# Kernel optimization log

Hardware: AMD Instinct MI355X
Metric: run time of the kernel (lower is better)

## Reference

```python
import jax, jax.numpy as jnp
import numpy as np

N = 50000          # nodes
E = 1_600_000      # edges (avg degree 32)
IN_CH = 256
HID = 256          # 2 * out_channels
OUT_CH = 128


def setup_inputs() -> dict:
    key = jax.random.key(0)
    k = jax.random.split(key, 5)
    x = jax.random.normal(k[0], (N, IN_CH), dtype=jnp.float32)
    edge_index = jax.random.randint(k[1], (2, E), 0, N, dtype=jnp.int64)
    W1 = jax.random.normal(k[2], (IN_CH, HID), dtype=jnp.float32) * 0.05
    b1 = jnp.zeros((HID,), dtype=jnp.float32)
    W2 = jax.random.normal(k[3], (HID, OUT_CH), dtype=jnp.float32) * 0.05
    b2 = jnp.zeros((OUT_CH,), dtype=jnp.float32)
    return {"x": x, "edge_index": edge_index, "W1": W1, "b1": b1, "W2": W2, "b2": b2}


def _gcn_conv(x, src, dst, deg_inv_sqrt, W, b, n_nodes):
    # GCNConv: linear transform, then normalized sum-aggregation over edges
    # (edge list already includes self-loops; deg_inv_sqrt precomputed).
    h = x @ W                                   # [N, F_out]
    norm = deg_inv_sqrt[src] * deg_inv_sqrt[dst]  # [E+N]
    msg = h[src] * norm[:, None]                # gather + scale
    out = jax.ops.segment_sum(msg, dst, num_segments=n_nodes)  # scatter-add
    return out + b


def reference(x, edge_index, W1, b1, W2, b2):
    n = x.shape[0]
    loop = jnp.arange(n, dtype=edge_index.dtype)
    src = jnp.concatenate([edge_index[0], loop])   # with self-loops
    dst = jnp.concatenate([edge_index[1], loop])
    # symmetric degree normalization (edge weight 1, deg over targets)
    deg = jax.ops.segment_sum(jnp.ones_like(dst, dtype=x.dtype), dst, num_segments=n)
    deg_inv_sqrt = jnp.where(deg > 0, jax.lax.rsqrt(deg), 0.0)

    z = _gcn_conv(x, src, dst, deg_inv_sqrt, W1, b1, n)
    z = jax.nn.relu(z)
    z = _gcn_conv(z, src, dst, deg_inv_sqrt, W2, b2, n)

    # decode: gather endpoint embeddings of original edges, dot product
    value = jnp.sum(z[edge_index[0]] * z[edge_index[1]], axis=-1)  # [E]
    return value.reshape(-1)
```

## Files before the change

### kernel.cpp

```cpp
#include <hip/hip_runtime.h>

#define WS_ALIGN(x) (((x) + 255) & ~(size_t)255)

typedef float f4v __attribute__((ext_vector_type(4)));
__device__ inline void nt_store4(float* p, float4 v) {
  __builtin_nontemporal_store(*(f4v*)&v, (f4v*)p);
}

__global__ void k_init_deg(int* deg, int N) {
  int i = blockIdx.x * blockDim.x + threadIdx.x;
  if (i < N) deg[i] = 1;
}

__global__ void k_count(const int* __restrict__ dst, int E, int* __restrict__ deg) {
  int e = blockIdx.x * blockDim.x + threadIdx.x;
  if (e < E) atomicAdd(&deg[dst[e]], 1);
}

__global__ void k_dis(const int* __restrict__ deg, float* __restrict__ dis, int N) {
  int i = blockIdx.x * blockDim.x + threadIdx.x;
  if (i < N) dis[i] = rsqrtf((float)deg[i]);
}

__global__ __launch_bounds__(1024) void k_scan(const int* __restrict__ deg,
                                               int* __restrict__ rowptr,
                                               int* __restrict__ cursor,
                                               int N, int Etot) {
  __shared__ int wsum[16];
  __shared__ int s_carry;
  int tid = threadIdx.x, lane = tid & 63, w = tid >> 6;
  if (tid == 0) { s_carry = 0; rowptr[N] = Etot; }
  __syncthreads();
  for (int base = 0; base < N; base += 4096) {
    int i0 = base + tid * 4;
    int v[4];
    #pragma unroll
    for (int u = 0; u < 4; ++u) {
      int i = i0 + u;
      v[u] = (i < N) ? (deg[i] - 1) : 0;
    }
    int tsum = v[0] + v[1] + v[2] + v[3];
    int sc = tsum;
    #pragma unroll
    for (int off = 1; off < 64; off <<= 1) {
      int t = __shfl_up(sc, off);
      if (lane >= off) sc += t;
    }
    if (lane == 63) wsum[w] = sc;
    __syncthreads();
    if (w == 0 && lane < 16) {
      int xx = wsum[lane];
      #pragma unroll
      for (int off = 1; off < 16; off <<= 1) {
        int t = __shfl_up(xx, off);
        if (lane >= off) xx += t;
      }
      wsum[lane] = xx;
    }
    __syncthreads();
    int woff = (w == 0) ? 0 : wsum[w - 1];
    int excl = s_carry + woff + (sc - tsum);
    #pragma unroll
    for (int u = 0; u < 4; ++u) {
      int i = i0 + u;
      if (i < N) { rowptr[i] = excl; cursor[i] = excl; }
      excl += v[u];
    }
    __syncthreads();
    if (tid == 0) s_carry += wsum[15];
    __syncthreads();
  }
}

__global__ void k_fill_pack(const int* __restrict__ src, const int* __restrict__ dst, int E,
                            int* __restrict__ cursor, unsigned short* __restrict__ csr16,
                            unsigned int* __restrict__ packed) {
  int e = blockIdx.x * blockDim.x + threadIdx.x;
  if (e < E) {
    int s = src[e];
    int d = dst[e];
    packed[e] = (unsigned int)s | ((unsigned int)d << 16);
    int pos = atomicAdd(&cursor[d], 1);
    csr16[pos] = (unsigned short)s;
  }
}

#define BM 128
#define BN 128
#define BK 16
__global__ __launch_bounds__(256) void k_gemm_scale_sm(const float* __restrict__ A,
                                                       const float* __restrict__ B,
                                                       const float* __restrict__ dis,
                                                       float* __restrict__ C,
                                                       int M, int Nc, int K) {
  __shared__ float As[BK][BM];
  __shared__ float Bs[BK][BN];
  int tid = threadIdx.x;
  int block_row = blockIdx.x * BM;
  int block_col = blockIdx.y * BN;
  int tr = (tid >> 4) << 3;
  int tc = (tid & 15) << 3;
  float acc[8][8] = {};
  for (int k0 = 0; k0 < K; k0 += BK) {
    for (int t = tid; t < BM * BK / 4; t += 256) {
      int r = t >> 2;
      int cc = (t & 3) << 2;
      int gr = block_row + r;
      float4 v = {0.f, 0.f, 0.f, 0.f};
      if (gr < M) v = *(const float4*)(A + (size_t)gr * K + k0 + cc);
      As[cc + 0][r] = v.x; As[cc + 1][r] = v.y; As[cc + 2][r] = v.z; As[cc + 3][r] = v.w;
    }
    for (int t = tid; t < BK * BN / 4; t += 256) {
      int r = t >> 5;
      int cc = (t & 31) << 2;
      *(float4*)&Bs[r][cc] = *(const float4*)(B + (size_t)(k0 + r) * Nc + block_col + cc);
    }
    __syncthreads();
    #pragma unroll
    for (int k = 0; k < BK; ++k) {
      float a[8], b[8];
      *(float4*)&a[0] = *(const float4*)&As[k][tr];
      *(float4*)&a[4] = *(const float4*)&As[k][tr + 4];
      *(float4*)&b[0] = *(const float4*)&Bs[k][tc];
      *(float4*)&b[4] = *(const float4*)&Bs[k][tc + 4];
      #pragma unroll
      for (int i = 0; i < 8; ++i)
        #pragma unroll
        for (int j = 0; j < 8; ++j)
          acc[i][j] = fmaf(a[i], b[j], acc[i][j]);
    }
    __syncthreads();
  }
  int col0 = block_col + tc;
  size_t base = ((size_t)(col0 >> 4) * M) * 16 + (col0 & 15);
  for (int i = 0; i < 8; ++i) {
    int gr = block_row + tr + i;
    if (gr >= M) break;
    float s = dis[gr];
    float4 v0 = {acc[i][0] * s, acc[i][1] * s, acc[i][2] * s, acc[i][3] * s};
    float4 v1 = {acc[i][4] * s, acc[i][5] * s, acc[i][6] * s, acc[i][7] * s};
    float* cp = C + base + (size_t)gr * 16;
    *(float4*)cp = v0;
    *(float4*)(cp + 4) = v1;
  }
}

template <int FCH, bool OUTSLICE>
__global__ __launch_bounds__(256) void k_agg_xcd(const float* __restrict__ hs,
                                                 const int* __restrict__ rowptr,
                                                 const unsigned short* __restrict__ csr,
                                                 const float* __restrict__ dis,
                                                 const float* __restrict__ bias,
                                                 float* __restrict__ out,
                                                 int N, int do_relu) {
  const int NSLICE = FCH / 16;
  int bid = blockIdx.x;
  int xcd = bid & 7;
  int wid = threadIdx.x >> 6;
  int lane = threadIdx.x & 63;
  int sub = lane >> 3;
  int epar = (lane >> 2) & 1;
  int c2 = lane & 3;
  int wix = ((bid >> 3) << 2) + wid;
  int wpx = ((int)(gridDim.x >> 3)) << 2;
  int nchunk = (N + 7) >> 3;

  for (int ph = 0; ph < NSLICE / 8; ++ph) {
    int s = xcd + (ph << 3);
    const float* in = hs + (size_t)s * N * 16;
    for (int ch = wix; ch < nchunk; ch += wpx) {
      int node = (ch << 3) + sub;
      bool valid = node < N;
      int b0 = 0, e0 = 0;
      if (valid) { b0 = rowptr[node]; e0 = rowptr[node + 1]; }
      float4 acc = {0.f, 0.f, 0.f, 0.f};
      int j = b0 + epar;
      for (; j + 6 < e0; j += 8) {
        int i0 = csr[j];     int i1 = csr[j + 2];
        int i2 = csr[j + 4]; int i3 = csr[j + 6];
        float4 v0 = *(const float4*)(in + ((size_t)i0 << 4) + (c2 << 2));
        float4 v1 = *(const float4*)(in + ((size_t)i1 << 4) + (c2 << 2));
        float4 v2 = *(const float4*)(in + ((size_t)i2 << 4) + (c2 << 2));
        float4 v3 = *(const float4*)(in + ((size_t)i3 << 4) + (c2 << 2));
        acc.x += (v0.x + v1.x) + (v2.x + v3.x);
        acc.y += (v0.y + v1.y) + (v2.y + v3.y);
        acc.z += (v0.z + v1.z) + (v2.z + v3.z);
        acc.w += (v0.w + v1.w) + (v2.w + v3.w);
      }
      for (; j < e0; j += 2) {
        int idx = csr[j];
        float4 v = *(const float4*)(in + ((size_t)idx << 4) + (c2 << 2));
        acc.x += v.x; acc.y += v.y; acc.z += v.z; acc.w += v.w;
      }
      acc.x += __shfl_xor(acc.x, 4);
      acc.y += __shfl_xor(acc.y, 4);
      acc.z += __shfl_xor(acc.z, 4);
      acc.w += __shfl_xor(acc.w, 4);
      if (valid && epar == 0) {
        float4 self = *(const float4*)(in + ((size_t)node << 4) + (c2 << 2));
        float dn = dis[node];
        int col = (s << 4) + (c2 << 2);
        float4 bv = *(const float4*)(bias + col);
        float4 r;
        r.x = (acc.x + self.x) * dn + bv.x;
        r.y = (acc.y + self.y) * dn + bv.y;
        r.z = (acc.z + self.z) * dn + bv.z;
        r.w = (acc.w + self.w) * dn + bv.w;
        if (do_relu) {
          r.x = fmaxf(r.x, 0.f); r.y = fmaxf(r.y, 0.f);
          r.z = fmaxf(r.z, 0.f); r.w = fmaxf(r.w, 0.f);
        }
        if (OUTSLICE)
          nt_store4(out + (size_t)s * N * 16 + ((size_t)node << 4) + (c2 << 2), r);
        else
          nt_store4(out + (size_t)node * FCH + col, r);
      }
    }
  }
}

__global__ __launch_bounds__(256) void k_decode_xcd4(const float* __restrict__ z,
                                                     const unsigned int* __restrict__ packed,
                                                     float* __restrict__ partial,
                                                     int E, int N) {
  int bid = blockIdx.x;
  int xcd = bid & 7;
  int wid = threadIdx.x >> 6;
  int lane = threadIdx.x & 63;
  int c2 = lane & 3;
  int sub = lane >> 2;
  int wix = ((bid >> 3) << 2) + wid;
  int wpx = ((int)(gridDim.x >> 3)) << 2;
  const float* zc = z + (size_t)xcd * N * 16;
  float* pp = partial + (size_t)xcd * E;

  for (int e0 = wix * 32; e0 < E; e0 += wpx * 32) {
    int eA = e0 + sub;
    int eB = e0 + 16 + sub;
    bool vA = eA < E, vB = eB < E;
    unsigned int pkA = 0, pkB = 0;
    if (vA) pkA = packed[eA];
    if (vB) pkB = packed[eB];
    float pA = 0.f, pB = 0.f;
    if (vA) {
      int a = (int)(pkA & 0xFFFFu), d = (int)(pkA >> 16);
      float4 za = *(const float4*)(zc + ((size_t)a << 4) + (c2 << 2));
      float4 zb = *(const float4*)(zc + ((size_t)d << 4) + (c2 << 2));
      pA = za.x * zb.x + za.y * zb.y + za.z * zb.z + za.w * zb.w;
    }
    if (vB) {
      int a = (int)(pkB & 0xFFFFu), d = (int)(pkB >> 16);
      float4 za = *(const float4*)(zc + ((size_t)a << 4) + (c2 << 2));
      float4 zb = *(const float4*)(zc + ((size_t)d << 4) + (c2 << 2));
      pB = za.x * zb.x + za.y * zb.y + za.z * zb.z + za.w * zb.w;
    }
    pA += __shfl_xor(pA, 1);
    pA += __shfl_xor(pA, 2);
    pB += __shfl_xor(pB, 1);
    pB += __shfl_xor(pB, 2);
    if (c2 == 0) {
      if (vA) pp[eA] = pA;
      if (vB) pp[eB] = pB;
    }
  }
}

__global__ void k_dreduce(const float* __restrict__ partial, float* __restrict__ out, int E) {
  int e = blockIdx.x * 256 + threadIdx.x;
  if (e >= E) return;
  float s = 0.f;
  #pragma unroll
  for (int k = 0; k < 8; ++k) s += partial[(size_t)k * E + e];
  out[e] = s;
}

extern "C" void kernel_launch(void* const* d_in, const int* in_sizes, int n_in,
                              void* d_out, int out_size, void* d_ws, size_t ws_size,
                              hipStream_t stream) {
  const float* x  = (const float*)d_in[0];
  const int* eidx = (const int*)d_in[1];
  const float* W1 = (const float*)d_in[2];
  const float* b1 = (const float*)d_in[3];
  const float* W2 = (const float*)d_in[4];
  const float* b2 = (const float*)d_in[5];
  float* out = (float*)d_out;

  const int IN_CH = 256, HID = 256, OUT_CH = 128;
  const int N = in_sizes[0] / IN_CH;
  const int E = in_sizes[1] / 2;
  const int* esrc = eidx;
  const int* edst = eidx + E;

  char* p = (char*)d_ws;
  auto alloc = [&](size_t bytes) -> char* { char* r = p; p += WS_ALIGN(bytes); return r; };
  int*   deg    = (int*)  alloc(sizeof(int) * N);
  float* dis    = (float*)alloc(sizeof(float) * N);
  int*   rowptr = (int*)  alloc(sizeof(int) * (N + 1));
  int*   cursor = (int*)  alloc(sizeof(int) * N);
  unsigned short* csr16 = (unsigned short*)alloc(sizeof(unsigned short) * (size_t)E);
  unsigned int*   packed = (unsigned int*) alloc(sizeof(unsigned int) * (size_t)E);
  float* bufA   = (float*)alloc(sizeof(float) * (size_t)N * HID);
  float* bufB   = (float*)alloc(sizeof(float) * (size_t)N * HID);

  const int T = 256;
  hipLaunchKernelGGL(k_init_deg, dim3((N + T - 1) / T), dim3(T), 0, stream, deg, N);
  hipLaunchKernelGGL(k_count, dim3((E + T - 1) / T), dim3(T), 0, stream, edst, E, deg);
  hipLaunchKernelGGL(k_dis, dim3((N + T - 1) / T), dim3(T), 0, stream, deg, dis, N);
  hipLaunchKernelGGL(k_scan, dim3(1), dim3(1024), 0, stream, deg, rowptr, cursor, N, E);
  hipLaunchKernelGGL(k_fill_pack, dim3((E + T - 1) / T), dim3(T), 0, stream,
                     esrc, edst, E, cursor, csr16, packed);

  const int PG = 2048;

  dim3 g1((N + BM - 1) / BM, HID / BN);
  hipLaunchKernelGGL(k_gemm_scale_sm, g1, dim3(256), 0, stream, x, W1, dis, bufA, N, HID, IN_CH);
  hipLaunchKernelGGL((k_agg_xcd<256, false>), dim3(PG), dim3(256), 0, stream,
                     bufA, rowptr, csr16, dis, b1, bufB, N, 1);

  dim3 g2((N + BM - 1) / BM, OUT_CH / BN);
  hipLaunchKernelGGL(k_gemm_scale_sm, g2, dim3(256), 0, stream, bufB, W2, dis, bufA, N, OUT_CH, HID);
  hipLaunchKernelGGL((k_agg_xcd<128, true>), dim3(PG), dim3(256), 0, stream,
                     bufA, rowptr, csr16, dis, b2, bufB, N, 0);

  hipLaunchKernelGGL(k_decode_xcd4, dim3(PG), dim3(256), 0, stream,
                     bufB, packed, bufA, E, N);
  hipLaunchKernelGGL(k_dreduce, dim3((E + 255) / 256), dim3(256), 0, stream,
                     bufA, out, E);
}
```

Before: 783.2 us.

## Deepen gather unrolling, batch decode edges, vectorize reduce, memset degree init

Adds a 16-edge unrolled gather loop in the aggregation kernel and makes the decode kernel handle four edge groups per iteration. Both changes put more independent loads in flight per wave. The partial-sum reduction now uses float4 loads and stores, four edges per thread. The degree-init kernel becomes a memset, with the self-loop +1 moved into the rsqrt and scan. The wider unrolls raise register pressure and may reduce occupancy.

```diff
diff --git a/kernel.cpp b/kernel.cpp
--- a/kernel.cpp
+++ b/kernel.cpp
@@ -7,11 +7,6 @@
   __builtin_nontemporal_store(*(f4v*)&v, (f4v*)p);
 }
 
-__global__ void k_init_deg(int* deg, int N) {
-  int i = blockIdx.x * blockDim.x + threadIdx.x;
-  if (i < N) deg[i] = 1;
-}
-
 __global__ void k_count(const int* __restrict__ dst, int E, int* __restrict__ deg) {
   int e = blockIdx.x * blockDim.x + threadIdx.x;
   if (e < E) atomicAdd(&deg[dst[e]], 1);
@@ -19,7 +14,7 @@
 
 __global__ void k_dis(const int* __restrict__ deg, float* __restrict__ dis, int N) {
   int i = blockIdx.x * blockDim.x + threadIdx.x;
-  if (i < N) dis[i] = rsqrtf((float)deg[i]);
+  if (i < N) dis[i] = rsqrtf((float)(deg[i] + 1));
 }
 
 __global__ __launch_bounds__(1024) void k_scan(const int* __restrict__ deg,
@@ -37,7 +32,7 @@
     #pragma unroll
     for (int u = 0; u < 4; ++u) {
       int i = i0 + u;
-      v[u] = (i < N) ? (deg[i] - 1) : 0;
+      v[u] = (i < N) ? deg[i] : 0;
     }
     int tsum = v[0] + v[1] + v[2] + v[3];
     int sc = tsum;
@@ -175,6 +170,24 @@
       if (valid) { b0 = rowptr[node]; e0 = rowptr[node + 1]; }
       float4 acc = {0.f, 0.f, 0.f, 0.f};
       int j = b0 + epar;
+      for (; j + 14 < e0; j += 16) {
+        int i0 = csr[j];      int i1 = csr[j + 2];
+        int i2 = csr[j + 4];  int i3 = csr[j + 6];
+        int i4 = csr[j + 8];  int i5 = csr[j + 10];
+        int i6 = csr[j + 12]; int i7 = csr[j + 14];
+        float4 v0 = *(const float4*)(in + ((size_t)i0 << 4) + (c2 << 2));
+        float4 v1 = *(const float4*)(in + ((size_t)i1 << 4) + (c2 << 2));
+        float4 v2 = *(const float4*)(in + ((size_t)i2 << 4) + (c2 << 2));
+        float4 v3 = *(const float4*)(in + ((size_t)i3 << 4) + (c2 << 2));
+        float4 v4 = *(const float4*)(in + ((size_t)i4 << 4) + (c2 << 2));
+        float4 v5 = *(const float4*)(in + ((size_t)i5 << 4) + (c2 << 2));
+        float4 v6 = *(const float4*)(in + ((size_t)i6 << 4) + (c2 << 2));
+        float4 v7 = *(const float4*)(in + ((size_t)i7 << 4) + (c2 << 2));
+        acc.x += ((v0.x + v1.x) + (v2.x + v3.x)) + ((v4.x + v5.x) + (v6.x + v7.x));
+        acc.y += ((v0.y + v1.y) + (v2.y + v3.y)) + ((v4.y + v5.y) + (v6.y + v7.y));
+        acc.z += ((v0.z + v1.z) + (v2.z + v3.z)) + ((v4.z + v5.z) + (v6.z + v7.z));
+        acc.w += ((v0.w + v1.w) + (v2.w + v3.w)) + ((v4.w + v5.w) + (v6.w + v7.w));
+      }
       for (; j + 6 < e0; j += 8) {
         int i0 = csr[j];     int i1 = csr[j + 2];
         int i2 = csr[j + 4]; int i3 = csr[j + 6];
@@ -234,44 +247,55 @@
   const float* zc = z + (size_t)xcd * N * 16;
   float* pp = partial + (size_t)xcd * E;
 
-  for (int e0 = wix * 32; e0 < E; e0 += wpx * 32) {
-    int eA = e0 + sub;
-    int eB = e0 + 16 + sub;
-    bool vA = eA < E, vB = eB < E;
-    unsigned int pkA = 0, pkB = 0;
-    if (vA) pkA = packed[eA];
-    if (vB) pkB = packed[eB];
-    float pA = 0.f, pB = 0.f;
-    if (vA) {
-      int a = (int)(pkA & 0xFFFFu), d = (int)(pkA >> 16);
-      float4 za = *(const float4*)(zc + ((size_t)a << 4) + (c2 << 2));
-      float4 zb = *(const float4*)(zc + ((size_t)d << 4) + (c2 << 2));
-      pA = za.x * zb.x + za.y * zb.y + za.z * zb.z + za.w * zb.w;
-    }
-    if (vB) {
-      int a = (int)(pkB & 0xFFFFu), d = (int)(pkB >> 16);
-      float4 za = *(const float4*)(zc + ((size_t)a << 4) + (c2 << 2));
-      float4 zb = *(const float4*)(zc + ((size_t)d << 4) + (c2 << 2));
-      pB = za.x * zb.x + za.y * zb.y + za.z * zb.z + za.w * zb.w;
-    }
-    pA += __shfl_xor(pA, 1);
-    pA += __shfl_xor(pA, 2);
-    pB += __shfl_xor(pB, 1);
-    pB += __shfl_xor(pB, 2);
+  for (int e0 = wix * 64; e0 < E; e0 += wpx * 64) {
+    float pv[4];
+    int ev[4];
+    #pragma unroll
+    for (int q = 0; q < 4; ++q) {
+      int e = e0 + q * 16 + sub;
+      ev[q] = e;
+      pv[q] = 0.f;
+      if (e < E) {
+        unsigned int pk = packed[e];
+        int a = (int)(pk & 0xFFFFu), d = (int)(pk >> 16);
+        float4 za = *(const float4*)(zc + ((size_t)a << 4) + (c2 << 2));
+        float4 zb = *(const float4*)(zc + ((size_t)d << 4) + (c2 << 2));
+        pv[q] = za.x * zb.x + za.y * zb.y + za.z * zb.z + za.w * zb.w;
+      }
+    }
+    #pragma unroll
+    for (int q = 0; q < 4; ++q) {
+      pv[q] += __shfl_xor(pv[q], 1);
+      pv[q] += __shfl_xor(pv[q], 2);
+    }
     if (c2 == 0) {
-      if (vA) pp[eA] = pA;
-      if (vB) pp[eB] = pB;
-    }
-  }
-}
-
-__global__ void k_dreduce(const float* __restrict__ partial, float* __restrict__ out, int E) {
-  int e = blockIdx.x * 256 + threadIdx.x;
+      #pragma unroll
+      for (int q = 0; q < 4; ++q)
+        if (ev[q] < E) pp[ev[q]] = pv[q];
+    }
+  }
+}
+
+__global__ void k_dreduce4(const float* __restrict__ partial, float* __restrict__ out, int E) {
+  int q = blockIdx.x * 256 + threadIdx.x;
+  int e = q << 2;
   if (e >= E) return;
-  float s = 0.f;
-  #pragma unroll
-  for (int k = 0; k < 8; ++k) s += partial[(size_t)k * E + e];
-  out[e] = s;
+  if (e + 4 <= E) {
+    float4 s = *(const float4*)(partial + e);
+    #pragma unroll
+    for (int k = 1; k < 8; ++k) {
+      float4 t = *(const float4*)(partial + (size_t)k * E + e);
+      s.x += t.x; s.y += t.y; s.z += t.z; s.w += t.w;
+    }
+    *(float4*)(out + e) = s;
+  } else {
+    for (int i = e; i < E; ++i) {
+      float s = 0.f;
+      #pragma unroll
+      for (int k = 0; k < 8; ++k) s += partial[(size_t)k * E + i];
+      out[i] = s;
+    }
+  }
 }
 
 extern "C" void kernel_launch(void* const* d_in, const int* in_sizes, int n_in,
@@ -303,7 +327,7 @@
   float* bufB   = (float*)alloc(sizeof(float) * (size_t)N * HID);
 
   const int T = 256;
-  hipLaunchKernelGGL(k_init_deg, dim3((N + T - 1) / T), dim3(T), 0, stream, deg, N);
+  hipMemsetAsync(deg, 0, sizeof(int) * N, stream);
   hipLaunchKernelGGL(k_count, dim3((E + T - 1) / T), dim3(T), 0, stream, edst, E, deg);
   hipLaunchKernelGGL(k_dis, dim3((N + T - 1) / T), dim3(T), 0, stream, deg, dis, N);
   hipLaunchKernelGGL(k_scan, dim3(1), dim3(1024), 0, stream, deg, rowptr, cursor, N, E);
@@ -324,6 +348,6 @@
 
   hipLaunchKernelGGL(k_decode_xcd4, dim3(PG), dim3(256), 0, stream,
                      bufB, packed, bufA, E, N);
-  hipLaunchKernelGGL(k_dreduce, dim3((E + 255) / 256), dim3(256), 0, stream,
+  hipLaunchKernelGGL(k_dreduce4, dim3((E / 4 + 255) / 256), dim3(256), 0, stream,
                      bufA, out, E);
 }
```

Result: no change. 790.3 us (+0.9%).
